# Optimization experiments

Measured on AMD Instinct MI355X. Metric: run time of the kernel, lower is better.

The kernel has to match this reference:

```python
import jax, jax.numpy as jnp
import numpy as np

B, S, D, H = 4, 2048, 1024, 16
DH = D // H


def _rope_tables():
    # standard RoPE angle tables, shaped [1, S, 1, DH] as the module expects
    inv_freq = 1.0 / (10000.0 ** (np.arange(0, DH, 2, dtype=np.float32) / DH))
    ang = np.arange(S, dtype=np.float32)[:, None] * inv_freq[None, :]  # [S, DH/2]
    ang = np.concatenate([ang, ang], axis=-1)  # [S, DH]
    cos = jnp.asarray(np.cos(ang))[None, :, None, :]
    sin = jnp.asarray(np.sin(ang))[None, :, None, :]
    return cos, sin


def setup_inputs() -> dict:
    key = jax.random.key(0)
    ks = jax.random.split(key, 5)
    x = jax.random.normal(ks[0], (B, S, D), dtype=jnp.float32)
    wq = jax.random.normal(ks[1], (D, D), dtype=jnp.float32) * 0.02
    wk = jax.random.normal(ks[2], (D, D), dtype=jnp.float32) * 0.02
    wv = jax.random.normal(ks[3], (D, D), dtype=jnp.float32) * 0.02
    wo = jax.random.normal(ks[4], (D, D), dtype=jnp.float32) * 0.02
    cos, sin = _rope_tables()
    return {"x": x, "cos": cos, "sin": sin, "wq": wq, "wk": wk, "wv": wv, "wo": wo}


def _rotate_half(t):
    t1, t2 = t[..., : DH // 2], t[..., DH // 2:]
    return jnp.concatenate([-t2, t1], axis=-1)


def reference(x, cos, sin, wq, wk, wv, wo):
    b, s, d = x.shape
    # QKV projections (torch Linear: y = x @ W.T), reshape to [B, H, S, DH]
    q = (x @ wq.T).reshape(b, s, H, DH).transpose(0, 2, 1, 3)
    k = (x @ wk.T).reshape(b, s, H, DH).transpose(0, 2, 1, 3)
    v = (x @ wv.T).reshape(b, s, H, DH).transpose(0, 2, 1, 3)
    # permute(0,2,1,3): [1,S,1,DH] -> [1,1,S,DH]; slice [:, :s] is a no-op on the size-1 head dim
    cos_p = jnp.transpose(cos, (0, 2, 1, 3))[:, :s]
    sin_p = jnp.transpose(sin, (0, 2, 1, 3))[:, :s]
    q = q * cos_p + _rotate_half(q) * sin_p
    k = k * cos_p + _rotate_half(k) * sin_p
    # SDPA (no mask, dropout_p = 0)
    scores = jnp.einsum("bhqd,bhkd->bhqk", q, k) / jnp.sqrt(jnp.float32(DH))
    attn = jax.nn.softmax(scores, axis=-1)
    out = jnp.einsum("bhqk,bhkd->bhqd", attn, v)
    out = out.transpose(0, 2, 1, 3).reshape(b, s, d)
    return out @ wo.T
```

## Files before the change

### kernel.cpp

```cpp
#include <hip/hip_runtime.h>
#include <hip/hip_bf16.h>
#include <stdint.h>

#define B 4
#define S 2048
#define D 1024
#define H 16
#define DH 64
#define M_TOT (B*S)
#define BH (B*H)

typedef unsigned short u16;
typedef unsigned int u32;
typedef __attribute__((ext_vector_type(4))) float f32x4;
typedef __attribute__((ext_vector_type(16))) float f32x16;
typedef __attribute__((ext_vector_type(8))) short bf16x8;
typedef __attribute__((ext_vector_type(2))) unsigned int u32x2;

typedef const __attribute__((address_space(1))) unsigned int* gp_t;
typedef __attribute__((address_space(3))) unsigned int* lp_t;

__device__ __forceinline__ void gload_lds16(const void* g, void* l) {
    __builtin_amdgcn_global_load_lds((gp_t)g, (lp_t)l, 16, 0, 0);
}

__device__ __forceinline__ float bf2f(u16 u) {
    u32 t = ((u32)u) << 16;
    float f; __builtin_memcpy(&f, &t, 4); return f;
}
__device__ __forceinline__ u16 f2bf(float f) {
    u32 u; __builtin_memcpy(&u, &f, 4);
    u += 0x7fffu + ((u >> 16) & 1u);
    return (u16)(u >> 16);
}
__device__ __forceinline__ u32 packbf(float lo, float hi_) {
    __hip_bfloat162 h = __float22bfloat162_rn(float2{lo, hi_});
    u32 r; __builtin_memcpy(&r, &h, 4); return r;
}

__device__ __forceinline__ float exp2_fast(float x) { return __builtin_amdgcn_exp2f(x); }

#if __has_builtin(__builtin_amdgcn_permlane32_swap)
__device__ __forceinline__ void plswap(u32& a, u32& bb) {
    u32x2 r = __builtin_amdgcn_permlane32_swap(a, bb, false, false);
    a = r.x; bb = r.y;
}
#else
__device__ __forceinline__ void plswap(u32& a, u32& bb) {
    int hi = (threadIdx.x >> 5) & 1;
    u32 ra = (u32)__shfl_xor((int)a, 32);
    u32 rb = (u32)__shfl_xor((int)bb, 32);
    u32 na = hi ? rb : a;
    u32 nb = hi ? bb : ra;
    a = na; bb = nb;
}
#endif

__global__ __launch_bounds__(256)
void cvt_all_kernel(const float* __restrict__ x,
                    const float* __restrict__ wq, const float* __restrict__ wk,
                    const float* __restrict__ wv, const float* __restrict__ wo,
                    u16* __restrict__ xb, u16* __restrict__ wqb, u16* __restrict__ wkb,
                    u16* __restrict__ wvb, u16* __restrict__ wob)
{
    const size_t MD = (size_t)M_TOT * D;
    const size_t WD = (size_t)D * D;
    size_t i = ((size_t)blockIdx.x * 256 + threadIdx.x) * 8;
    const float* src; u16* dst; size_t off;
    if (i < MD) { src = x; dst = xb; off = i; }
    else {
        size_t j = i - MD;
        int wsel = (int)(j >> 20);
        off = j & (WD - 1);
        if      (wsel == 0) { src = wq; dst = wqb; }
        else if (wsel == 1) { src = wk; dst = wkb; }
        else if (wsel == 2) { src = wv; dst = wvb; }
        else                { src = wo; dst = wob; }
    }
    float4 a = *(const float4*)(src + off);
    float4 b = *(const float4*)(src + off + 4);
    union { u16 u[8]; bf16x8 v; } o;
    o.u[0] = f2bf(a.x); o.u[1] = f2bf(a.y); o.u[2] = f2bf(a.z); o.u[3] = f2bf(a.w);
    o.u[4] = f2bf(b.x); o.u[5] = f2bf(b.y); o.u[6] = f2bf(b.z); o.u[7] = f2bf(b.w);
    *(bf16x8*)(dst + off) = o.v;
}

template<int WRITE_BF16, int DO_ROPE>
__global__ __launch_bounds__(256)
void gemm_mfma(const u16* __restrict__ X,
               const u16* __restrict__ W0, const u16* __restrict__ W1, const u16* __restrict__ W2,
               void* Y0, void* Y1, void* Y2,
               const float* __restrict__ cosT, const float* __restrict__ sinT)
{
    __shared__ __align__(16) u16 Al[128 * 32];
    __shared__ __align__(16) u16 Bl[128 * 32];

    const u16* Wm = (blockIdx.z == 0) ? W0 : (blockIdx.z == 1) ? W1 : W2;
    void* Yv      = (blockIdx.z == 0) ? Y0 : (blockIdx.z == 1) ? Y1 : Y2;

    const int t = threadIdx.x;
    const int w = t >> 6, ll = t & 63;
    const int wr = w >> 1, wc = w & 1;
    const int g = ll >> 4, lc = ll & 15;
    const int m0 = blockIdx.x * 128, n0 = blockIdx.y * 128;

    const int srow = t >> 2;
    const int scol = (t & 3) * 8;

    const u16* Xa = X + (size_t)m0 * D;
    const u16* Wa = Wm + (size_t)n0 * D;

    f32x4 acc[4][4];
    #pragma unroll
    for (int i = 0; i < 4; ++i)
        #pragma unroll
        for (int j = 0; j < 4; ++j)
            acc[i][j] = (f32x4){0.f, 0.f, 0.f, 0.f};

    for (int k0 = 0; k0 < D; k0 += 32) {
        gload_lds16(Xa + (size_t)(srow)      * D + k0 + scol, &Al[(w * 64) * 8]);
        gload_lds16(Xa + (size_t)(64 + srow) * D + k0 + scol, &Al[(256 + w * 64) * 8]);
        gload_lds16(Wa + (size_t)(srow)      * D + k0 + scol, &Bl[(w * 64) * 8]);
        gload_lds16(Wa + (size_t)(64 + srow) * D + k0 + scol, &Bl[(256 + w * 64) * 8]);
        __syncthreads();

        bf16x8 af[4], bf[4];
        #pragma unroll
        for (int i = 0; i < 4; ++i)
            af[i] = *(const bf16x8*)&Al[(wr * 64 + i * 16 + lc) * 32 + g * 8];
        #pragma unroll
        for (int j = 0; j < 4; ++j)
            bf[j] = *(const bf16x8*)&Bl[(wc * 64 + j * 16 + lc) * 32 + g * 8];

        #pragma unroll
        for (int i = 0; i < 4; ++i)
            #pragma unroll
            for (int j = 0; j < 4; ++j)
                acc[i][j] = __builtin_amdgcn_mfma_f32_16x16x32_bf16(af[i], bf[j], acc[i][j], 0, 0, 0);
        __syncthreads();
    }

    if (DO_ROPE && blockIdx.z < 2) {
        const float scale = (blockIdx.z == 0) ? (0.125f * 1.44269504f) : 1.0f;
        u16* Y = (u16*)Yv;
        #pragma unroll
        for (int i = 0; i < 4; ++i)
            #pragma unroll
            for (int r = 0; r < 4; ++r) {
                int row = m0 + wr * 64 + i * 16 + g * 4 + r;
                int s = row & (S - 1);
                #pragma unroll
                for (int jh = 0; jh < 2; ++jh) {
                    float c  = cosT[s * DH + jh * 16 + lc];
                    float sn = sinT[s * DH + jh * 16 + lc];
                    float a0 = acc[i][jh][r], a1 = acc[i][jh + 2][r];
                    size_t base = (size_t)row * D + n0 + wc * 64;
                    Y[base + jh * 16 + lc]       = f2bf((a0 * c - a1 * sn) * scale);
                    Y[base + (jh + 2) * 16 + lc] = f2bf((a1 * c + a0 * sn) * scale);
                }
            }
    } else if (DO_ROPE) {
        u16* Y = (u16*)Yv;
        #pragma unroll
        for (int i = 0; i < 4; ++i)
            #pragma unroll
            for (int j = 0; j < 4; ++j) {
                int row = m0 + wr * 64 + i * 16 + g * 4;
                int col = n0 + wc * 64 + j * 16 + lc;
                int bt = row >> 11, s = row & (S - 1);
                size_t vtrow = (size_t)(bt * 16 + (col >> 6)) * 64 + (col & 63);
                u32 w0 = packbf(acc[i][j][0], acc[i][j][1]);
                u32 w1 = packbf(acc[i][j][2], acc[i][j][3]);
                u32x2 pr; pr.x = w0; pr.y = w1;
                *(u32x2*)&Y[vtrow * S + s] = pr;
            }
    } else if (WRITE_BF16) {
        u16* Y = (u16*)Yv;
        #pragma unroll
        for (int i = 0; i < 4; ++i)
            #pragma unroll
            for (int j = 0; j < 4; ++j)
                #pragma unroll
                for (int r = 0; r < 4; ++r) {
                    int row = m0 + wr * 64 + i * 16 + g * 4 + r;
                    int col = n0 + wc * 64 + j * 16 + lc;
                    Y[(size_t)row * D + col] = f2bf(acc[i][j][r]);
                }
    } else {
        float* Y = (float*)Yv;
        #pragma unroll
        for (int i = 0; i < 4; ++i)
            #pragma unroll
            for (int j = 0; j < 4; ++j)
                #pragma unroll
                for (int r = 0; r < 4; ++r) {
                    int row = m0 + wr * 64 + i * 16 + g * 4 + r;
                    int col = n0 + wc * 64 + j * 16 + lc;
                    Y[(size_t)row * D + col] = acc[i][j][r];
                }
    }
}

#define QBLK 256
#define KVT 128
#define NT (S / KVT)

__global__ __launch_bounds__(512, 2)
void attn_mfma(const u16* __restrict__ Q, const u16* __restrict__ Kg,
               const u16* __restrict__ Vt, u16* __restrict__ CTX)
{
    __shared__ __align__(16) u16 smem[32768];

    const int t   = threadIdx.x;
    const int w   = t >> 6;
    const int wq4 = w & 3;
    const int kh  = w >> 2;
    const int ll  = t & 63;
    const int q   = t & 31;
    const int hi  = (t >> 5) & 1;

    const int bid  = blockIdx.x;
    const int xcd  = bid & 7;
    const int slot = bid >> 3;
    const int bh   = xcd * 8 + (slot >> 3);
    const int qb   = slot & 7;
    const int b = bh >> 4, h = bh & 15;
    const int q0 = qb * QBLK;
    const int qbase = q0 + wq4 * 64;

    bf16x8 qf[2][4];
    #pragma unroll
    for (int qg = 0; qg < 2; ++qg) {
        const u16* qp = &Q[(size_t)(b*S + qbase + qg*32 + q) * D + h*DH + hi*8];
        qf[qg][0] = *(const bf16x8*)(qp);
        qf[qg][1] = *(const bf16x8*)(qp + 16);
        qf[qg][2] = *(const bf16x8*)(qp + 32);
        qf[qg][3] = *(const bf16x8*)(qp + 48);
    }

    f32x16 po[4], zv;
    float ls0 = 0.f, ls1 = 0.f;
    #pragma unroll
    for (int i = 0; i < 16; ++i) {
        po[0][i] = 0.f; po[1][i] = 0.f; po[2][i] = 0.f; po[3][i] = 0.f;
        zv[i] = 0.f;
    }

    const int ksrow = t >> 3;
    const int kscol = (((t & 7) << 4) ^ ((ksrow & 7) << 4)) >> 1;
    const int vsrow = t >> 4;
    const int vscol = (((t & 15) ^ (vsrow & 15)) << 3);
    const int rsw  = (q & 7) << 4;
    const int vsw  = (q & 15) << 4;

    u16* buf0 = smem;
    u16* buf1 = smem + 16384;

    const u16* kg = Kg + ((size_t)(b * S) + ksrow) * D + (size_t)h * DH + kscol;
    const u16* vg = Vt + ((size_t)bh * DH + vsrow) * S + vscol;

    #define STAGE(dst) do {                                  \
        gload_lds16(kg,          (dst) + w*512);             \
        gload_lds16(kg + 64*D,   (dst) + 4096 + w*512);      \
        gload_lds16(vg,          (dst) + 8192 + w*512);      \
        gload_lds16(vg + 32*S,   (dst) + 8192 + 4096 + w*512); \
        kg += (size_t)KVT * D; vg += KVT; } while (0)

    const int kh2 = kh * 2;
    auto compute = [&](const u16* base) {
        const u16* Kl = base;
        const u16* Vl = base + 8192;
        #pragma unroll
        for (int c = 0; c < 2; ++c) {
            const int ca = kh2 + c;
            f32x16 p0, p1;
            {
                const u16* kr = &Kl[(ca*32 + q) << 6];
                bf16x8 k0 = *(const bf16x8*)&kr[((0*32 + hi*16) ^ rsw) >> 1];
                p0 = __builtin_amdgcn_mfma_f32_32x32x16_bf16(k0, qf[0][0], zv, 0, 0, 0);
                p1 = __builtin_amdgcn_mfma_f32_32x32x16_bf16(k0, qf[1][0], zv, 0, 0, 0);
                #pragma unroll
                for (int cc = 1; cc < 4; ++cc) {
                    bf16x8 kf = *(const bf16x8*)&kr[((cc*32 + hi*16) ^ rsw) >> 1];
                    p0 = __builtin_amdgcn_mfma_f32_32x32x16_bf16(kf, qf[0][cc], p0, 0, 0, 0);
                    p1 = __builtin_amdgcn_mfma_f32_32x32x16_bf16(kf, qf[1][cc], p1, 0, 0, 0);
                }
            }

            u32 W0[8], W1[8];
            #pragma unroll
            for (int j = 0; j < 8; ++j) {
                float a0 = exp2_fast(p0[2*j]),  b0 = exp2_fast(p0[2*j + 1]);
                float a1 = exp2_fast(p1[2*j]),  b1 = exp2_fast(p1[2*j + 1]);
                ls0 += a0 + b0;
                ls1 += a1 + b1;
                W0[j] = packbf(a0, b0);
                W1[j] = packbf(a1, b1);
            }
            plswap(W0[0], W0[2]); plswap(W0[1], W0[3]);
            plswap(W0[4], W0[6]); plswap(W0[5], W0[7]);
            plswap(W1[0], W1[2]); plswap(W1[1], W1[3]);
            plswap(W1[4], W1[6]); plswap(W1[5], W1[7]);
            bf16x8 pa0a, pa0b, pa1a, pa1b;
            {
                union { u32 u[4]; bf16x8 v; } pb;
                pb.u[0]=W0[0]; pb.u[1]=W0[1]; pb.u[2]=W0[2]; pb.u[3]=W0[3]; pa0a = pb.v;
                pb.u[0]=W0[4]; pb.u[1]=W0[5]; pb.u[2]=W0[6]; pb.u[3]=W0[7]; pa0b = pb.v;
                pb.u[0]=W1[0]; pb.u[1]=W1[1]; pb.u[2]=W1[2]; pb.u[3]=W1[3]; pa1a = pb.v;
                pb.u[0]=W1[4]; pb.u[1]=W1[5]; pb.u[2]=W1[6]; pb.u[3]=W1[7]; pa1b = pb.v;
            }

            #pragma unroll
            for (int kk = 0; kk < 2; ++kk) {
                int vb = ((ca*64 + kk*32 + hi*16) ^ vsw) >> 1;
                bf16x8 v0 = *(const bf16x8*)&Vl[(q << 7) + vb];
                bf16x8 v1 = *(const bf16x8*)&Vl[((32 + q) << 7) + vb];
                bf16x8 pq0 = kk ? pa0b : pa0a;
                bf16x8 pq1 = kk ? pa1b : pa1a;
                po[0] = __builtin_amdgcn_mfma_f32_32x32x16_bf16(v0, pq0, po[0], 0, 0, 0);
                po[1] = __builtin_amdgcn_mfma_f32_32x32x16_bf16(v1, pq0, po[1], 0, 0, 0);
                po[2] = __builtin_amdgcn_mfma_f32_32x32x16_bf16(v0, pq1, po[2], 0, 0, 0);
                po[3] = __builtin_amdgcn_mfma_f32_32x32x16_bf16(v1, pq1, po[3], 0, 0, 0);
            }
        }
    };

    STAGE(buf0);
    asm volatile("s_waitcnt vmcnt(0)" ::: "memory");
    __builtin_amdgcn_s_barrier();

    for (int ti = 0; ti < NT; ti += 2) {
        STAGE(buf1);
        compute(buf0);
        asm volatile("s_waitcnt vmcnt(0)" ::: "memory");
        __builtin_amdgcn_s_barrier();
        if (ti < NT - 2) STAGE(buf0);
        compute(buf1);
        asm volatile("s_waitcnt vmcnt(0)" ::: "memory");
        __builtin_amdgcn_s_barrier();
    }
    #undef STAGE

    float* cb = (float*)smem;
    if (kh == 1) {
        #pragma unroll
        for (int i = 0; i < 16; ++i) {
            cb[wq4*2048 + i*64 + ll]        = po[0][i];
            cb[wq4*2048 + (16+i)*64 + ll]   = po[1][i];
        }
        cb[8192 + 0*256 + wq4*64 + ll] = ls0;
        cb[8192 + 1*256 + wq4*64 + ll] = ls1;
    }
    __syncthreads();
    if (kh == 0) {
        #pragma unroll
        for (int i = 0; i < 16; ++i) {
            po[0][i] += cb[wq4*2048 + i*64 + ll];
            po[1][i] += cb[wq4*2048 + (16+i)*64 + ll];
        }
        ls0 += cb[8192 + 0*256 + wq4*64 + ll];
        ls1 += cb[8192 + 1*256 + wq4*64 + ll];
    }
    __syncthreads();
    if (kh == 1) {
        #pragma unroll
        for (int i = 0; i < 16; ++i) {
            cb[wq4*2048 + i*64 + ll]        = po[2][i];
            cb[wq4*2048 + (16+i)*64 + ll]   = po[3][i];
        }
    }
    __syncthreads();
    if (kh == 0) {
        #pragma unroll
        for (int i = 0; i < 16; ++i) {
            po[2][i] += cb[wq4*2048 + i*64 + ll];
            po[3][i] += cb[wq4*2048 + (16+i)*64 + ll];
        }
    }
    __syncthreads();

    if (kh == 0) {
        float lst[2];
        lst[0] = ls0 + __shfl_xor(ls0, 32);
        lst[1] = ls1 + __shfl_xor(ls1, 32);
        u16* ow = &smem[wq4 * 2304];
        #pragma unroll
        for (int qg = 0; qg < 2; ++qg) {
            float inv = 1.f / lst[qg];
            #pragma unroll
            for (int r = 0; r < 16; ++r) {
                int d0 = (r & 3) + 8 * (r >> 2) + 4 * hi;
                ow[q * 72 + d0]      = f2bf(po[qg*2 + 0][r] * inv);
                ow[q * 72 + 32 + d0] = f2bf(po[qg*2 + 1][r] * inv);
            }
            int row = ll >> 1, half = t & 1;
            const u16* orow = &ow[row * 72 + half * 32];
            u16* gp = &CTX[(size_t)(b*S + qbase + qg*32 + row) * D + h*DH + half * 32];
            #pragma unroll
            for (int i = 0; i < 4; ++i)
                *(bf16x8*)(gp + i * 8) = *(const bf16x8*)(orow + i * 8);
        }
    }
}

extern "C" void kernel_launch(void* const* d_in, const int* in_sizes, int n_in,
                              void* d_out, int out_size, void* d_ws, size_t ws_size,
                              hipStream_t stream)
{
    const float* x    = (const float*)d_in[0];
    const float* cosT = (const float*)d_in[1];
    const float* sinT = (const float*)d_in[2];
    const float* wq   = (const float*)d_in[3];
    const float* wk   = (const float*)d_in[4];
    const float* wv   = (const float*)d_in[5];
    const float* wo   = (const float*)d_in[6];
    float* out = (float*)d_out;

    const size_t MD = (size_t)M_TOT * D;
    const size_t WD = (size_t)D * D;

    u16* xb   = (u16*)d_ws;
    u16* Qb   = xb + MD;
    u16* Kb   = Qb + MD;
    u16* Vtb  = Kb + MD;
    u16* CTXb = Vtb + MD;
    u16* wqb  = CTXb + MD;
    u16* wkb  = wqb + WD;
    u16* wvb  = wkb + WD;
    u16* wob  = wvb + WD;

    cvt_all_kernel<<<(int)((MD + 4*WD) / 8 / 256), 256, 0, stream>>>(
        x, wq, wk, wv, wo, xb, wqb, wkb, wvb, wob);

    gemm_mfma<1, 1><<<dim3(M_TOT / 128, D / 128, 3), 256, 0, stream>>>(
        xb, wqb, wkb, wvb, Qb, Kb, Vtb, cosT, sinT);

    attn_mfma<<<dim3(M_TOT / QBLK * H), 512, 0, stream>>>(Qb, Kb, Vtb, CTXb);

    gemm_mfma<0, 0><<<dim3(M_TOT / 128, D / 128, 1), 256, 0, stream>>>(
        CTXb, wob, nullptr, nullptr, out, nullptr, nullptr, nullptr, nullptr);
}
```

Before: 186.8 us.

## Load K and V fragments directly from global memory instead of LDS staging

Removes the double-buffered LDS staging of K/V tiles with async global-to-LDS loads and per-tile barriers. Each wave now reads its K and V MFMA fragments straight from global memory, relying on L2/L1 caching for reuse across the four query waves. This eliminates barriers and LDS traffic and shrinks shared memory to the reduction buffer. In exchange, each wave issues its own redundant global loads with no explicit prefetch, so load latency is exposed in the loop.

```diff
diff --git a/kernel.cpp b/kernel.cpp
--- a/kernel.cpp
+++ b/kernel.cpp
@@ -202,14 +202,12 @@
 }
 
 #define QBLK 256
-#define KVT 128
-#define NT (S / KVT)
 
 __global__ __launch_bounds__(512, 2)
 void attn_mfma(const u16* __restrict__ Q, const u16* __restrict__ Kg,
                const u16* __restrict__ Vt, u16* __restrict__ CTX)
 {
-    __shared__ __align__(16) u16 smem[32768];
+    __shared__ float cb[8704];
 
     const int t   = threadIdx.x;
     const int w   = t >> 6;
@@ -246,46 +244,28 @@
         zv[i] = 0.f;
     }
 
-    const int ksrow = t >> 3;
-    const int kscol = (((t & 7) << 4) ^ ((ksrow & 7) << 4)) >> 1;
-    const int vsrow = t >> 4;
-    const int vscol = (((t & 15) ^ (vsrow & 15)) << 3);
-    const int rsw  = (q & 7) << 4;
-    const int vsw  = (q & 15) << 4;
-
-    u16* buf0 = smem;
-    u16* buf1 = smem + 16384;
-
-    const u16* kg = Kg + ((size_t)(b * S) + ksrow) * D + (size_t)h * DH + kscol;
-    const u16* vg = Vt + ((size_t)bh * DH + vsrow) * S + vscol;
-
-    #define STAGE(dst) do {                                  \
-        gload_lds16(kg,          (dst) + w*512);             \
-        gload_lds16(kg + 64*D,   (dst) + 4096 + w*512);      \
-        gload_lds16(vg,          (dst) + 8192 + w*512);      \
-        gload_lds16(vg + 32*S,   (dst) + 8192 + 4096 + w*512); \
-        kg += (size_t)KVT * D; vg += KVT; } while (0)
-
-    const int kh2 = kh * 2;
-    auto compute = [&](const u16* base) {
-        const u16* Kl = base;
-        const u16* Vl = base + 8192;
+    const u16* krow = Kg + ((size_t)(b*S) + q) * D + h*DH + hi*8;
+    const u16* vr0  = Vt + ((size_t)bh*DH + q)      * S + hi*8;
+    const u16* vr1  = Vt + ((size_t)bh*DH + 32 + q) * S + hi*8;
+
+    for (int ko = kh*64; ko < S; ko += 128) {
         #pragma unroll
         for (int c = 0; c < 2; ++c) {
-            const int ca = kh2 + c;
+            const int ck = ko + c*32;
+            const u16* kr = krow + (size_t)ck * D;
+            bf16x8 kf0 = *(const bf16x8*)(kr);
+            bf16x8 kf1 = *(const bf16x8*)(kr + 16);
+            bf16x8 kf2 = *(const bf16x8*)(kr + 32);
+            bf16x8 kf3 = *(const bf16x8*)(kr + 48);
             f32x16 p0, p1;
-            {
-                const u16* kr = &Kl[(ca*32 + q) << 6];
-                bf16x8 k0 = *(const bf16x8*)&kr[((0*32 + hi*16) ^ rsw) >> 1];
-                p0 = __builtin_amdgcn_mfma_f32_32x32x16_bf16(k0, qf[0][0], zv, 0, 0, 0);
-                p1 = __builtin_amdgcn_mfma_f32_32x32x16_bf16(k0, qf[1][0], zv, 0, 0, 0);
-                #pragma unroll
-                for (int cc = 1; cc < 4; ++cc) {
-                    bf16x8 kf = *(const bf16x8*)&kr[((cc*32 + hi*16) ^ rsw) >> 1];
-                    p0 = __builtin_amdgcn_mfma_f32_32x32x16_bf16(kf, qf[0][cc], p0, 0, 0, 0);
-                    p1 = __builtin_amdgcn_mfma_f32_32x32x16_bf16(kf, qf[1][cc], p1, 0, 0, 0);
-                }
-            }
+            p0 = __builtin_amdgcn_mfma_f32_32x32x16_bf16(kf0, qf[0][0], zv, 0, 0, 0);
+            p1 = __builtin_amdgcn_mfma_f32_32x32x16_bf16(kf0, qf[1][0], zv, 0, 0, 0);
+            p0 = __builtin_amdgcn_mfma_f32_32x32x16_bf16(kf1, qf[0][1], p0, 0, 0, 0);
+            p1 = __builtin_amdgcn_mfma_f32_32x32x16_bf16(kf1, qf[1][1], p1, 0, 0, 0);
+            p0 = __builtin_amdgcn_mfma_f32_32x32x16_bf16(kf2, qf[0][2], p0, 0, 0, 0);
+            p1 = __builtin_amdgcn_mfma_f32_32x32x16_bf16(kf2, qf[1][2], p1, 0, 0, 0);
+            p0 = __builtin_amdgcn_mfma_f32_32x32x16_bf16(kf3, qf[0][3], p0, 0, 0, 0);
+            p1 = __builtin_amdgcn_mfma_f32_32x32x16_bf16(kf3, qf[1][3], p1, 0, 0, 0);
 
             u32 W0[8], W1[8];
             #pragma unroll
@@ -312,9 +292,8 @@
 
             #pragma unroll
             for (int kk = 0; kk < 2; ++kk) {
-                int vb = ((ca*64 + kk*32 + hi*16) ^ vsw) >> 1;
-                bf16x8 v0 = *(const bf16x8*)&Vl[(q << 7) + vb];
-                bf16x8 v1 = *(const bf16x8*)&Vl[((32 + q) << 7) + vb];
+                bf16x8 v0 = *(const bf16x8*)(vr0 + ck + kk*16);
+                bf16x8 v1 = *(const bf16x8*)(vr1 + ck + kk*16);
                 bf16x8 pq0 = kk ? pa0b : pa0a;
                 bf16x8 pq1 = kk ? pa1b : pa1a;
                 po[0] = __builtin_amdgcn_mfma_f32_32x32x16_bf16(v0, pq0, po[0], 0, 0, 0);
@@ -323,25 +302,9 @@
                 po[3] = __builtin_amdgcn_mfma_f32_32x32x16_bf16(v1, pq1, po[3], 0, 0, 0);
             }
         }
-    };
-
-    STAGE(buf0);
-    asm volatile("s_waitcnt vmcnt(0)" ::: "memory");
-    __builtin_amdgcn_s_barrier();
-
-    for (int ti = 0; ti < NT; ti += 2) {
-        STAGE(buf1);
-        compute(buf0);
-        asm volatile("s_waitcnt vmcnt(0)" ::: "memory");
-        __builtin_amdgcn_s_barrier();
-        if (ti < NT - 2) STAGE(buf0);
-        compute(buf1);
-        asm volatile("s_waitcnt vmcnt(0)" ::: "memory");
-        __builtin_amdgcn_s_barrier();
-    }
-    #undef STAGE
-
-    float* cb = (float*)smem;
+    }
+
+    __syncthreads();
     if (kh == 1) {
         #pragma unroll
         for (int i = 0; i < 16; ++i) {
@@ -383,7 +346,7 @@
         float lst[2];
         lst[0] = ls0 + __shfl_xor(ls0, 32);
         lst[1] = ls1 + __shfl_xor(ls1, 32);
-        u16* ow = &smem[wq4 * 2304];
+        u16* ow = (u16*)cb + wq4 * 2304;
         #pragma unroll
         for (int qg = 0; qg < 2; ++qg) {
             float inv = 1.f / lst[qg];
```

Measured after the change: 229.6 us. 22.9% more time.
